# Kernel optimization log

Hardware: AMD Instinct MI355X
Metric: run time of the kernel (lower is better)

The kernel has to match this reference:

```python
import jax, jax.numpy as jnp
import numpy as np
from itertools import product

L0 = (41, 1600, 1408)  # sparse_shape (z,y,x) from pc_range / voxel_size + [1,0,0]
B = 4
N_PER = 25000
PNAMES = ['w_in','s_in','b_in','w1','s1','b1','w2a','s2a','b2a','w2b','s2b','b2b','w2c','s2c','b2c','w3a','s3a','b3a','w3b','s3b','b3b','w3c','s3c','b3c','w4a','s4a','b4a','w4b','s4b','b4b','w4c','s4c','b4c','w_out','s_out','b_out']


def _enc(c, shape):
    D, H, W = shape
    return ((c[:, 0].astype(np.int64) * D + c[:, 1]) * H + c[:, 2]) * W + c[:, 3]


def _subm_rb(coords, shape):
    # submanifold conv rulebook: out site i gathers input j with coord_j = coord_i + offset
    N = coords.shape[0]
    keys = _enc(coords, shape)
    order = np.argsort(keys); sk = keys[order]
    ins, outs = [], []
    for dz, dy, dx in product((-1, 0, 1), repeat=3):
        nb = coords.astype(np.int64).copy()
        nb[:, 1] += dz; nb[:, 2] += dy; nb[:, 3] += dx
        ok = ((nb[:, 1] >= 0) & (nb[:, 1] < shape[0]) & (nb[:, 2] >= 0) & (nb[:, 2] < shape[1]) & (nb[:, 3] >= 0) & (nb[:, 3] < shape[2]))
        qi = np.nonzero(ok)[0]
        qk = _enc(nb[qi], shape)
        pos = np.clip(np.searchsorted(sk, qk), 0, N - 1)
        f = sk[pos] == qk
        ins.append(order[pos[f]].astype(np.int32))
        outs.append(qi[f].astype(np.int32))
    R = max(len(a) for a in ins)
    rin = np.zeros((27, R), np.int32); rout = np.full((27, R), N, np.int32)  # pad -> dummy out row
    for k in range(27):
        rin[k, :len(ins[k])] = ins[k]; rout[k, :len(outs[k])] = outs[k]
    return jnp.asarray(rin), jnp.asarray(rout)


def _spconv_rb(coords, shape, ks, st, pd):
    # strided sparse conv: out = (in + pad - k) / stride where divisible and in-bounds
    osh = tuple((shape[i] + 2 * pd[i] - ks[i]) // st[i] + 1 for i in range(3))
    per = []; allk = []
    for off in product(*[range(k) for k in ks]):
        oc = np.empty((coords.shape[0], 4), np.int64)
        oc[:, 0] = coords[:, 0]
        ok = np.ones(coords.shape[0], bool)
        for d in range(3):
            v = coords[:, d + 1].astype(np.int64) + pd[d] - off[d]
            ok &= (v % st[d] == 0)
            v = v // st[d]
            ok &= (v >= 0) & (v < osh[d])
            oc[:, d + 1] = v
        qi = np.nonzero(ok)[0]
        qk = _enc(oc[qi], osh)
        per.append((qi.astype(np.int32), qk)); allk.append(qk)
    uk = np.unique(np.concatenate(allk))
    Nout = len(uk); K = len(per)
    R = max(len(qi) for qi, _ in per)
    rin = np.zeros((K, R), np.int32); rout = np.full((K, R), Nout, np.int32)
    for k, (qi, qk) in enumerate(per):
        rin[k, :len(qi)] = qi
        rout[k, :len(qi)] = np.searchsorted(uk, qk).astype(np.int32)
    t = uk.copy()
    x = t % osh[2]; t //= osh[2]; y = t % osh[1]; t //= osh[1]; z = t % osh[0]; b = t // osh[0]
    ocoords = np.stack([b, z, y, x], 1).astype(np.int32)
    return jnp.asarray(rin), jnp.asarray(rout), ocoords, osh


def _gen_coords(rng):
    # clustered LiDAR-like voxel occupancy: gaussian clusters so 3x3x3 neighborhoods are populated
    out = []
    for b in range(B):
        nc = 250
        ctr = np.stack([rng.integers(6, 34, nc), rng.integers(60, 1540, nc), rng.integers(60, 1348, nc)], 1)
        pts = ctr[np.repeat(np.arange(nc), 400)] + rng.normal(0.0, 2.0, (nc * 400, 3))
        pts = np.rint(pts).astype(np.int64)
        for d in range(3):
            pts[:, d] = np.clip(pts[:, d], 0, L0[d] - 1)
        keys = (pts[:, 0] * L0[1] + pts[:, 1]) * L0[2] + pts[:, 2]
        _, ui = np.unique(keys, return_index=True)
        assert len(ui) >= N_PER
        c = pts[np.sort(ui[:N_PER])]
        out.append(np.concatenate([np.full((N_PER, 1), b, np.int64), c], 1))
    return np.concatenate(out, 0).astype(np.int32)


def _conv(feat, W, rin, rout, nout):
    # gather -> per-offset GEMM -> scatter-add (spconv rulebook algorithm)
    out = jnp.zeros((nout + 1, W.shape[2]), feat.dtype)  # +1 dummy row for padding
    for k in range(W.shape[0]):
        out = out.at[rout[k]].add(feat[rin[k]] @ W[k])
    return out[:nout]


def _bnrelu(x, s, b):
    # eval-mode BatchNorm1d folded to affine, then ReLU
    return jax.nn.relu(x * s + b)


def _net(voxels, normalizer, rb1_in, rb1_out, rb2s_in, rb2s_out, batch2, rb2_in, rb2_out, rb3s_in, rb3s_out, batch3, rb3_in, rb3_out, rb4s_in, rb4s_out, batch4, rb4_in, rb4_out, rbo_in, rbo_out, batch_out, P):
    n0 = voxels.shape[0]; n2 = batch2.shape[0]; n3 = batch3.shape[0]; n4 = batch4.shape[0]; no = batch_out.shape[0]
    f = voxels.sum(1) / normalizer  # mean VFE: (N0, 4)
    x = _bnrelu(_conv(f, P['w_in'], rb1_in, rb1_out, n0), P['s_in'], P['b_in'])
    x = _bnrelu(_conv(x, P['w1'], rb1_in, rb1_out, n0), P['s1'], P['b1'])
    x = _bnrelu(_conv(x, P['w2a'], rb2s_in, rb2s_out, n2), P['s2a'], P['b2a'])
    x = _bnrelu(_conv(x, P['w2b'], rb2_in, rb2_out, n2), P['s2b'], P['b2b'])
    x = _bnrelu(_conv(x, P['w2c'], rb2_in, rb2_out, n2), P['s2c'], P['b2c'])
    x = _bnrelu(_conv(x, P['w3a'], rb3s_in, rb3s_out, n3), P['s3a'], P['b3a'])
    x = _bnrelu(_conv(x, P['w3b'], rb3_in, rb3_out, n3), P['s3b'], P['b3b'])
    x = _bnrelu(_conv(x, P['w3c'], rb3_in, rb3_out, n3), P['s3c'], P['b3c'])
    x = _bnrelu(_conv(x, P['w4a'], rb4s_in, rb4s_out, n4), P['s4a'], P['b4a'])
    x = _bnrelu(_conv(x, P['w4b'], rb4_in, rb4_out, n4), P['s4b'], P['b4b'])
    x = _bnrelu(_conv(x, P['w4c'], rb4_in, rb4_out, n4), P['s4c'], P['b4c'])
    x = _bnrelu(_conv(x, P['w_out'], rbo_in, rbo_out, no), P['s_out'], P['b_out'])
    # per-batch global max pool over active voxels (== F.max_pool1d over voxel dim)
    return jax.ops.segment_max(x, batch_out.astype(jnp.int32), num_segments=B)


def setup_inputs():
    rng = np.random.default_rng(0)
    coords0 = _gen_coords(rng)
    rb1_in, rb1_out = _subm_rb(coords0, L0)
    rb2s_in, rb2s_out, c2, sh2 = _spconv_rb(coords0, L0, (3, 3, 3), (2, 2, 2), (1, 1, 1))
    rb2_in, rb2_out = _subm_rb(c2, sh2)
    rb3s_in, rb3s_out, c3, sh3 = _spconv_rb(c2, sh2, (3, 3, 3), (2, 2, 2), (1, 1, 1))
    rb3_in, rb3_out = _subm_rb(c3, sh3)
    rb4s_in, rb4s_out, c4, sh4 = _spconv_rb(c3, sh3, (3, 3, 3), (2, 2, 2), (0, 1, 1))
    rb4_in, rb4_out = _subm_rb(c4, sh4)
    rbo_in, rbo_out, co, _ = _spconv_rb(c4, sh4, (3, 1, 1), (2, 1, 1), (0, 0, 0))
    N0 = coords0.shape[0]
    d = dict(
        voxels=jnp.asarray(rng.normal(0, 1, (N0, 5, 4)).astype(np.float32)),
        voxel_num_points=jnp.asarray(rng.integers(1, 6, N0).astype(np.int32)),
        voxel_coords=jnp.asarray(coords0),
        rb1_in=rb1_in, rb1_out=rb1_out,
        rb2s_in=rb2s_in, rb2s_out=rb2s_out, batch2=jnp.asarray(c2[:, 0]),
        rb2_in=rb2_in, rb2_out=rb2_out,
        rb3s_in=rb3s_in, rb3s_out=rb3s_out, batch3=jnp.asarray(c3[:, 0]),
        rb3_in=rb3_in, rb3_out=rb3_out,
        rb4s_in=rb4s_in, rb4s_out=rb4s_out, batch4=jnp.asarray(c4[:, 0]),
        rb4_in=rb4_in, rb4_out=rb4_out,
        rbo_in=rbo_in, rbo_out=rbo_out, batch_out=jnp.asarray(co[:, 0]),
    )
    def _w(k, ci, co_):
        return jnp.asarray((rng.normal(0, 1, (k, ci, co_)) / np.sqrt(k * ci)).astype(np.float32))
    def _bn(c):
        return (jnp.asarray(rng.uniform(0.5, 1.5, c).astype(np.float32)), jnp.asarray(rng.normal(0, 0.1, c).astype(np.float32)))
    d['w_in'] = _w(27, 4, 16); d['s_in'], d['b_in'] = _bn(16)
    d['w1'] = _w(27, 16, 16); d['s1'], d['b1'] = _bn(16)
    d['w2a'] = _w(27, 16, 32); d['s2a'], d['b2a'] = _bn(32)
    d['w2b'] = _w(27, 32, 32); d['s2b'], d['b2b'] = _bn(32)
    d['w2c'] = _w(27, 32, 32); d['s2c'], d['b2c'] = _bn(32)
    d['w3a'] = _w(27, 32, 64); d['s3a'], d['b3a'] = _bn(64)
    d['w3b'] = _w(27, 64, 64); d['s3b'], d['b3b'] = _bn(64)
    d['w3c'] = _w(27, 64, 64); d['s3c'], d['b3c'] = _bn(64)
    d['w4a'] = _w(27, 64, 64); d['s4a'], d['b4a'] = _bn(64)
    d['w4b'] = _w(27, 64, 64); d['s4b'], d['b4b'] = _bn(64)
    d['w4c'] = _w(27, 64, 64); d['s4c'], d['b4c'] = _bn(64)
    d['w_out'] = _w(3, 64, 128); d['s_out'], d['b_out'] = _bn(128)
    return d


def reference(voxels, voxel_num_points, voxel_coords, rb1_in, rb1_out, rb2s_in, rb2s_out, batch2, rb2_in, rb2_out, rb3s_in, rb3s_out, batch3, rb3_in, rb3_out, rb4s_in, rb4s_out, batch4, rb4_in, rb4_out, rbo_in, rbo_out, batch_out, w_in, s_in, b_in, w1, s1, b1, w2a, s2a, b2a, w2b, s2b, b2b, w2c, s2c, b2c, w3a, s3a, b3a, w3b, s3b, b3b, w3c, s3c, b3c, w4a, s4a, b4a, w4b, s4b, b4b, w4c, s4c, b4c, w_out, s_out, b_out):
    normalizer = jnp.maximum(voxel_num_points.astype(voxels.dtype), 1.0)[:, None]
    P = dict(zip(PNAMES, (w_in, s_in, b_in, w1, s1, b1, w2a, s2a, b2a, w2b, s2b, b2b, w2c, s2c, b2c, w3a, s3a, b3a, w3b, s3b, b3b, w3c, s3c, b3c, w4a, s4a, b4a, w4b, s4b, b4b, w4c, s4c, b4c, w_out, s_out, b_out)))
    return _net(voxels, normalizer, rb1_in, rb1_out, rb2s_in, rb2s_out, batch2, rb2_in, rb2_out, rb3s_in, rb3s_out, batch3, rb3_in, rb3_out, rb4s_in, rb4s_out, batch4, rb4_in, rb4_out, rbo_in, rbo_out, batch_out, P)
```

## Files before the change

kernel.cpp:

```cpp
#include <hip/hip_runtime.h>
#include <cstddef>
#include <cstdint>

typedef _Float16 half8 __attribute__((ext_vector_type(8)));
typedef float floatx4 __attribute__((ext_vector_type(4)));

static inline int cdiv_i(int a, int b) { return (a + b - 1) / b; }

__global__ void feat_kernel(const float* __restrict__ vox,
                            const int* __restrict__ vnp,
                            _Float16* __restrict__ f, int N0) {
  int t = blockIdx.x * blockDim.x + threadIdx.x;
  if (t >= (N0 + 1) * 8) return;
  int i = t >> 3, c = t & 7;
  float v = 0.f;
  if (i < N0 && c < 4) {
    const float* p = vox + (size_t)i * 20 + c;
    v = (p[0] + p[4] + p[8] + p[12] + p[16]) / fmaxf((float)vnp[i], 1.f);
  }
  f[t] = (_Float16)v;
}

struct RB { const int* rin; const int* rout; int K, R, nout, start, end, off; };
struct RBs { RB d[8]; };
__global__ void rb_fill_all(RBs P, int* __restrict__ tbl, int total) {
  int idx = blockIdx.x * blockDim.x + threadIdx.x;
  if (idx >= total) return;
#pragma unroll
  for (int l = 0; l < 8; ++l) {
    if (idx >= P.d[l].start && idx < P.d[l].end) {
      const RB rb = P.d[l];
      int e = idx - rb.start;
      int o = rb.rout[e];
      if ((unsigned)o < (unsigned)rb.nout) {
        int k = e / rb.R;
        tbl[rb.off + (size_t)k * rb.nout + o] = rb.rin[e];
      }
    }
  }
}

__global__ void tbl_fill_kernel(const int* __restrict__ rin,
                                const int* __restrict__ rout,
                                int* __restrict__ tbl, int K, int R, int nout) {
  int e = blockIdx.x * blockDim.x + threadIdx.x;
  if (e >= K * R) return;
  int o = rout[e];
  if ((unsigned)o >= (unsigned)nout) return;
  int k = e / R;
  tbl[(size_t)k * nout + o] = rin[e];
}

struct WP { const float* W; int K, Ci, CiPad, Co, start, end, off; };
struct WPs { WP d[12]; };
__global__ void wpack_all(WPs P, _Float16* __restrict__ Bp, int total) {
  int idx = blockIdx.x * blockDim.x + threadIdx.x;
  if (idx >= total) return;
#pragma unroll
  for (int l = 0; l < 12; ++l) {
    if (idx >= P.d[l].start && idx < P.d[l].end) {
      const WP w = P.d[l];
      int e = idx - w.start;
      int j = e & 7;
      int lane = (e >> 3) & 63;
      int rest = e >> 9;
      int NT = w.Co >> 4;
      int t = rest % NT, ch = rest / NT;
      int kk = ch * 32 + ((lane >> 4) << 3) + j;
      int k = kk / w.CiPad, ci = kk % w.CiPad;
      int n = t * 16 + (lane & 15);
      float v = (k < w.K && ci < w.Ci)
                    ? w.W[((size_t)k * w.Ci + ci) * w.Co + n]
                    : 0.f;
      Bp[w.off + e] = (_Float16)v;
    }
  }
}

template <int K, int CiPad, int Co, int KS, int CG>
__global__ __launch_bounds__(256) void conv_mfma(
    const _Float16* __restrict__ feat, const _Float16* __restrict__ Bp,
    const int* __restrict__ tbl, const float* __restrict__ sc,
    const float* __restrict__ bi, _Float16* __restrict__ out,
    int nout, int nin) {
  constexpr int NT = Co / 16;
  constexpr int NTW = NT / CG;
  constexpr int RG = 4 / (KS * CG);
  static_assert(KS * CG * RG == 4 && RG >= 1 && NT % CG == 0);
  constexpr int DIV = (CiPad >= 32) ? (CiPad / 32) : 1;
  constexpr int NCH = (K * CiPad + 31) / 32;
  constexpr int L2C = (CiPad == 8) ? 3 : 4;
  constexpr int CoP = Co + 4;

  __shared__ float red[(KS > 1) ? (KS - 1) * RG * 16 * CoP : 1];

  if (blockIdx.x == 0 && threadIdx.x < Co)
    out[(size_t)nout * Co + threadIdx.x] = (_Float16)0.f;

  const int wave = threadIdx.x >> 6, lane = threadIdx.x & 63;
  const int ks = wave % KS;
  const int cg = (wave / KS) % CG;
  const int rowg = wave / (KS * CG);
  const int m = lane & 15, lb = (lane >> 4) * 8;
  const int i0 = (blockIdx.x * RG + rowg) * 16;
  if constexpr (KS == 1) {
    if (i0 >= nout) return;
  }
  const int row = i0 + m;
  const bool rOK = row < nout;

  floatx4 acc[NTW];
#pragma unroll
  for (int n = 0; n < NTW; ++n) {
    floatx4 z = {0.f, 0.f, 0.f, 0.f};
    acc[n] = z;
  }

  if constexpr (CiPad >= 32) {
    constexpr int NKW = (K + KS - 1) / KS;
    constexpr int NC = NKW * DIV;
    constexpr int DA = NC < 4 ? NC : 4;
    constexpr int DB = NC < 2 ? NC : 2;
    int idx[NKW];
#pragma unroll
    for (int q = 0; q < NKW; ++q) {
      int k = ks + q * KS;
      int jj = (rOK && k < K) ? tbl[(size_t)k * nout + row] : -1;
      idx[q] = (jj < 0) ? nin : jj;
    }
    half8 ap[DA];
    half8 bq[DB][NTW];
#pragma unroll
    for (int d = 0; d < DA; ++d)
      ap[d] = *(const half8*)(feat + (size_t)idx[d / DIV] * CiPad +
                              (d % DIV) * 32 + lb);
#pragma unroll
    for (int d = 0; d < DB; ++d) {
      int k = ks + (d / DIV) * KS;
      int ch = ((k < K) ? k : (K - 1)) * DIV + (d % DIV);
#pragma unroll
      for (int n = 0; n < NTW; ++n)
        bq[d][n] = *(const half8*)(Bp + ((size_t)ch * NT * 64 + lane) * 8 +
                                   (size_t)(cg * NTW + n) * 512);
    }
#pragma unroll
    for (int ii = 0; ii < NC; ++ii) {
      half8 a = ap[ii % DA];
      half8 bt[NTW];
#pragma unroll
      for (int n = 0; n < NTW; ++n) bt[n] = bq[ii % DB][n];
      if (ii + DA < NC) {
        int nx = ii + DA;
        ap[ii % DA] = *(const half8*)(feat + (size_t)idx[nx / DIV] * CiPad +
                                      (nx % DIV) * 32 + lb);
      }
      if (ii + DB < NC) {
        int nx = ii + DB;
        int k = ks + (nx / DIV) * KS;
        int ch = ((k < K) ? k : (K - 1)) * DIV + (nx % DIV);
#pragma unroll
        for (int n = 0; n < NTW; ++n)
          bq[ii % DB][n] = *(const half8*)(Bp + ((size_t)ch * NT * 64 + lane) * 8 +
                                           (size_t)(cg * NTW + n) * 512);
      }
#pragma unroll
      for (int n = 0; n < NTW; ++n)
        acc[n] = __builtin_amdgcn_mfma_f32_16x16x32_f16(a, bt[n], acc[n], 0, 0, 0);
    }
  } else {
    constexpr int NC = NCH;
    constexpr int DA = NC < 4 ? NC : 4;
    constexpr int DB = NC < 2 ? NC : 2;
    int idx[NC];
#pragma unroll
    for (int q = 0; q < NC; ++q) {
      int ko = (q * 32 + lb) >> L2C;
      int jj = (rOK && ko < K) ? tbl[(size_t)ko * nout + row] : -1;
      idx[q] = (jj < 0) ? nin : jj;
    }
    half8 ap[DA];
    half8 bq[DB][NTW];
#pragma unroll
    for (int d = 0; d < DA; ++d)
      ap[d] = *(const half8*)(feat + (size_t)idx[d] * CiPad +
                              ((d * 32 + lb) & (CiPad - 1)));
#pragma unroll
    for (int d = 0; d < DB; ++d)
#pragma unroll
      for (int n = 0; n < NTW; ++n)
        bq[d][n] = *(const half8*)(Bp + ((size_t)d * NT * 64 + lane) * 8 +
                                   (size_t)(cg * NTW + n) * 512);
#pragma unroll
    for (int ii = 0; ii < NC; ++ii) {
      half8 a = ap[ii % DA];
      half8 bt[NTW];
#pragma unroll
      for (int n = 0; n < NTW; ++n) bt[n] = bq[ii % DB][n];
      if (ii + DA < NC) {
        int nx = ii + DA;
        ap[ii % DA] = *(const half8*)(feat + (size_t)idx[nx] * CiPad +
                                      ((nx * 32 + lb) & (CiPad - 1)));
      }
      if (ii + DB < NC) {
        int nx = ii + DB;
#pragma unroll
        for (int n = 0; n < NTW; ++n)
          bq[ii % DB][n] = *(const half8*)(Bp + ((size_t)nx * NT * 64 + lane) * 8 +
                                           (size_t)(cg * NTW + n) * 512);
      }
#pragma unroll
      for (int n = 0; n < NTW; ++n)
        acc[n] = __builtin_amdgcn_mfma_f32_16x16x32_f16(a, bt[n], acc[n], 0, 0, 0);
    }
  }

  const int rl = (lane >> 4) * 4;
  if constexpr (KS > 1) {
    if (ks > 0) {
#pragma unroll
      for (int n = 0; n < NTW; ++n) {
        int col = (cg * NTW + n) * 16 + m;
#pragma unroll
        for (int r = 0; r < 4; ++r)
          red[((ks - 1) * RG + rowg) * 16 * CoP + (rl + r) * CoP + col] = acc[n][r];
      }
    }
    __syncthreads();
    if (ks > 0) return;
#pragma unroll
    for (int s = 1; s < KS; ++s)
#pragma unroll
      for (int n = 0; n < NTW; ++n) {
        int col = (cg * NTW + n) * 16 + m;
#pragma unroll
        for (int r = 0; r < 4; ++r)
          acc[n][r] += red[((s - 1) * RG + rowg) * 16 * CoP + (rl + r) * CoP + col];
      }
  }

#pragma unroll
  for (int n = 0; n < NTW; ++n) {
    int col = (cg * NTW + n) * 16 + m;
    float s_ = sc[col], b_ = bi[col];
#pragma unroll
    for (int r = 0; r < 4; ++r) {
      int orow = i0 + rl + r;
      if (orow < nout)
        out[(size_t)orow * Co + col] = (_Float16)fmaxf(fmaf(acc[n][r], s_, b_), 0.f);
    }
  }
}

__global__ __launch_bounds__(256) void segmax2(const _Float16* __restrict__ x,
                                               const int* __restrict__ batch,
                                               int n, float* __restrict__ out) {
  const int RPB = 128;
  int c = threadIdx.x & 127, g = threadIdx.x >> 7;
  int r0 = blockIdx.x * RPB + g;
  int rend = min(n, blockIdx.x * RPB + RPB);
  float mx = 0.f;
  int cb = -1;
  for (int r = r0; r < rend; r += 2) {
    int b = batch[r];
    if (b != cb) {
      if (cb >= 0)
        atomicMax((int*)out + ((size_t)cb << 7) + c, __float_as_int(mx));
      cb = b;
      mx = 0.f;
    }
    mx = fmaxf(mx, (float)x[(size_t)r * 128 + c]);
  }
  if (cb >= 0)
    atomicMax((int*)out + ((size_t)cb << 7) + c, __float_as_int(mx));
}

extern "C" void kernel_launch(void* const* d_in, const int* in_sizes, int n_in,
                              void* d_out, int out_size, void* d_ws, size_t ws_size,
                              hipStream_t stream) {
  auto I = [&](int idx) { return (const int*)d_in[idx]; };
  auto F = [&](int idx) { return (const float*)d_in[idx]; };

  const int N0  = in_sizes[1];
  const int R1  = in_sizes[3] / 27;
  const int R2s = in_sizes[5] / 27;
  const int n2  = in_sizes[7];
  const int R2  = in_sizes[8] / 27;
  const int R3s = in_sizes[10] / 27;
  const int n3  = in_sizes[12];
  const int R3  = in_sizes[13] / 27;
  const int R4s = in_sizes[15] / 27;
  const int n4  = in_sizes[17];
  const int R4  = in_sizes[18] / 27;
  const int Ro  = in_sizes[20] / 3;
  const int no  = in_sizes[22];

  const int wIdx[12] = {23, 26, 29, 32, 35, 38, 41, 44, 47, 50, 53, 56};
  const int Ks[12]   = {27, 27, 27, 27, 27, 27, 27, 27, 27, 27, 27, 3};
  const int Cis[12]  = {4, 16, 16, 32, 32, 32, 64, 64, 64, 64, 64, 64};
  const int Cos[12]  = {16, 16, 32, 32, 32, 64, 64, 64, 64, 64, 64, 128};
  WPs P;
  int wtot = 0;
  int bpOff[12];
  for (int l = 0; l < 12; ++l) {
    int cip = Cis[l] < 8 ? 8 : Cis[l];
    int nch = (Ks[l] * cip + 31) / 32;
    int nt = Cos[l] / 16;
    int sz = nch * nt * 512;
    P.d[l].W = F(wIdx[l]);
    P.d[l].K = Ks[l];  P.d[l].Ci = Cis[l];  P.d[l].CiPad = cip;  P.d[l].Co = Cos[l];
    P.d[l].start = wtot;  P.d[l].end = wtot + sz;  P.d[l].off = wtot;
    bpOff[l] = wtot;
    wtot += sz;
  }

  RBs RP;
  const int rbRin[8]  = {3, 5, 8, 10, 13, 15, 18, 20};
  const int rbRs[8]   = {R1, R2s, R2, R3s, R3, R4s, R4, Ro};
  const int rbKs[8]   = {27, 27, 27, 27, 27, 27, 27, 3};
  const int rbNout[8] = {N0, n2, n2, n3, n3, n4, n4, no};
  size_t tblInts[8];
  size_t tblOff[8];
  size_t totTbl = 0;
  int totFill = 0;
  for (int l = 0; l < 8; ++l) {
    tblInts[l] = (size_t)rbNout[l] * rbKs[l];
    tblOff[l] = totTbl;
    totTbl += tblInts[l];
    RP.d[l].rin = I(rbRin[l]);
    RP.d[l].rout = I(rbRin[l] + 1);
    RP.d[l].K = rbKs[l];  RP.d[l].R = rbRs[l];  RP.d[l].nout = rbNout[l];
    RP.d[l].start = totFill;
    totFill += rbKs[l] * rbRs[l];
    RP.d[l].end = totFill;
    RP.d[l].off = (int)tblOff[l];
  }

  size_t S = (size_t)(N0 + 1) * 16;
  auto smax = [&](size_t v) { if (v > S) S = v; };
  smax((size_t)(n2 + 1) * 32);
  smax((size_t)(n3 + 1) * 64);
  smax((size_t)(n4 + 1) * 64);
  smax((size_t)(no + 1) * 128);
  S = (S + 7) & ~(size_t)7;

  _Float16* h = (_Float16*)d_ws;
  size_t off = 0;
  _Float16* f0 = h + off;   off += (size_t)(N0 + 1) * 8;
  _Float16* bufA = h + off; off += S;
  _Float16* bufB = h + off; off += S;
  _Float16* Bp = h + off;   off += (size_t)((wtot + 7) & ~7);
  int* tblBase = (int*)(h + off);
  size_t usedBytes = off * 2;
  bool prebuilt = (usedBytes + totTbl * 4 <= ws_size);

  feat_kernel<<<cdiv_i((N0 + 1) * 8, 256), 256, 0, stream>>>(F(0), I(1), f0, N0);
  wpack_all<<<cdiv_i(wtot, 256), 256, 0, stream>>>(P, Bp, wtot);
  hipMemsetAsync(d_out, 0, (size_t)out_size * 4, stream);

  const int l2rb[12] = {0, 0, 1, 2, 2, 3, 4, 4, 5, 6, 6, 7};
  const int* tblL[12];
  if (prebuilt) {
    hipMemsetAsync(tblBase, 0xFF, totTbl * 4, stream);
    rb_fill_all<<<cdiv_i(totFill, 256), 256, 0, stream>>>(RP, tblBase, totFill);
    for (int l = 0; l < 12; ++l) tblL[l] = tblBase + tblOff[l2rb[l]];
  } else {
    for (int l = 0; l < 12; ++l) tblL[l] = tblBase;
  }
  auto buildSeq = [&](int rb) {
    if (prebuilt) return;
    hipMemsetAsync(tblBase, 0xFF, tblInts[rb] * 4, stream);
    tbl_fill_kernel<<<cdiv_i(rbKs[rb] * rbRs[rb], 256), 256, 0, stream>>>(
        I(rbRin[rb]), I(rbRin[rb] + 1), tblBase, rbKs[rb], rbRs[rb], rbNout[rb]);
  };

#define CONV(Kk, CIP, CO, KSv, CGv, IN, LI, OUTB, NOUT, NIN)                  \
  do {                                                                        \
    constexpr int rowsPerBlk = (4 / (KSv * CGv)) * 16;                        \
    conv_mfma<Kk, CIP, CO, KSv, CGv>                                          \
        <<<cdiv_i(NOUT, rowsPerBlk), 256, 0, stream>>>(                       \
            IN, Bp + bpOff[LI], tblL[LI], F(wIdx[LI] + 1), F(wIdx[LI] + 2),   \
            OUTB, NOUT, NIN);                                                 \
  } while (0)

  buildSeq(0);
  CONV(27, 8, 16, 1, 1, f0, 0, bufA, N0, N0);
  CONV(27, 16, 16, 1, 1, bufA, 1, bufB, N0, N0);
  buildSeq(1);
  CONV(27, 16, 32, 1, 1, bufB, 2, bufA, n2, N0);
  buildSeq(2);
  CONV(27, 32, 32, 1, 1, bufA, 3, bufB, n2, n2);
  CONV(27, 32, 32, 1, 1, bufB, 4, bufA, n2, n2);
  buildSeq(3);
  CONV(27, 32, 64, 2, 1, bufA, 5, bufB, n3, n2);
  buildSeq(4);
  CONV(27, 64, 64, 2, 1, bufB, 6, bufA, n3, n3);
  CONV(27, 64, 64, 2, 1, bufA, 7, bufB, n3, n3);
  buildSeq(5);
  CONV(27, 64, 64, 4, 1, bufB, 8, bufA, n4, n3);
  buildSeq(6);
  CONV(27, 64, 64, 4, 1, bufA, 9, bufB, n4, n4);
  CONV(27, 64, 64, 4, 1, bufB, 10, bufA, n4, n4);
  buildSeq(7);
  CONV(3, 64, 128, 2, 2, bufA, 11, bufB, no, n4);
  segmax2<<<cdiv_i(no, 128), 256, 0, stream>>>(bufB, I(22), no, (float*)d_out);
#undef CONV
}
```

Baseline: 464.0 us.

## Split conv work across K-slices and output-column blocks with XCD-aware block remap

```diff
diff --git a/kernel.cpp b/kernel.cpp
--- a/kernel.cpp
+++ b/kernel.cpp
@@ -77,37 +77,49 @@
   }
 }
 
-template <int K, int CiPad, int Co, int KS, int CG>
+template <int K, int CiPad, int Co, int KS, int CG, int CBLK>
 __global__ __launch_bounds__(256) void conv_mfma(
     const _Float16* __restrict__ feat, const _Float16* __restrict__ Bp,
     const int* __restrict__ tbl, const float* __restrict__ sc,
     const float* __restrict__ bi, _Float16* __restrict__ out,
     int nout, int nin) {
   constexpr int NT = Co / 16;
-  constexpr int NTW = NT / CG;
+  constexpr int NTE = NT / CBLK;
+  constexpr int NTW = NTE / CG;
   constexpr int RG = 4 / (KS * CG);
-  static_assert(KS * CG * RG == 4 && RG >= 1 && NT % CG == 0);
+  static_assert(KS * CG * RG == 4 && RG >= 1 && NT % CBLK == 0 && NTE % CG == 0);
   constexpr int DIV = (CiPad >= 32) ? (CiPad / 32) : 1;
   constexpr int NCH = (K * CiPad + 31) / 32;
   constexpr int L2C = (CiPad == 8) ? 3 : 4;
-  constexpr int CoP = Co + 4;
+  constexpr int CoP = NTE * 16 + 4;
 
   __shared__ float red[(KS > 1) ? (KS - 1) * RG * 16 * CoP : 1];
 
   if (blockIdx.x == 0 && threadIdx.x < Co)
     out[(size_t)nout * Co + threadIdx.x] = (_Float16)0.f;
+
+  int id = blockIdx.x;
+  {
+    int nb = gridDim.x, nb8 = (nb >> 3) << 3;
+    if (id < nb8) {
+      int per = nb >> 3;
+      id = (id & 7) * per + (id >> 3);
+    }
+  }
+  const int rt = id / CBLK, cb = id % CBLK;
 
   const int wave = threadIdx.x >> 6, lane = threadIdx.x & 63;
   const int ks = wave % KS;
   const int cg = (wave / KS) % CG;
   const int rowg = wave / (KS * CG);
   const int m = lane & 15, lb = (lane >> 4) * 8;
-  const int i0 = (blockIdx.x * RG + rowg) * 16;
+  const int i0 = (rt * RG + rowg) * 16;
   if constexpr (KS == 1) {
     if (i0 >= nout) return;
   }
   const int row = i0 + m;
   const bool rOK = row < nout;
+  const int ct0 = cb * NTE + cg * NTW;
 
   floatx4 acc[NTW];
 #pragma unroll
@@ -119,7 +131,7 @@
   if constexpr (CiPad >= 32) {
     constexpr int NKW = (K + KS - 1) / KS;
     constexpr int NC = NKW * DIV;
-    constexpr int DA = NC < 4 ? NC : 4;
+    constexpr int DA = NC < 8 ? NC : 8;
     constexpr int DB = NC < 2 ? NC : 2;
     int idx[NKW];
 #pragma unroll
@@ -141,7 +153,7 @@
 #pragma unroll
       for (int n = 0; n < NTW; ++n)
         bq[d][n] = *(const half8*)(Bp + ((size_t)ch * NT * 64 + lane) * 8 +
-                                   (size_t)(cg * NTW + n) * 512);
+                                   (size_t)(ct0 + n) * 512);
     }
 #pragma unroll
     for (int ii = 0; ii < NC; ++ii) {
@@ -161,52 +173,61 @@
 #pragma unroll
         for (int n = 0; n < NTW; ++n)
           bq[ii % DB][n] = *(const half8*)(Bp + ((size_t)ch * NT * 64 + lane) * 8 +
-                                           (size_t)(cg * NTW + n) * 512);
+                                           (size_t)(ct0 + n) * 512);
       }
 #pragma unroll
       for (int n = 0; n < NTW; ++n)
         acc[n] = __builtin_amdgcn_mfma_f32_16x16x32_f16(a, bt[n], acc[n], 0, 0, 0);
     }
   } else {
-    constexpr int NC = NCH;
-    constexpr int DA = NC < 4 ? NC : 4;
-    constexpr int DB = NC < 2 ? NC : 2;
-    int idx[NC];
-#pragma unroll
-    for (int q = 0; q < NC; ++q) {
-      int ko = (q * 32 + lb) >> L2C;
-      int jj = (rOK && ko < K) ? tbl[(size_t)ko * nout + row] : -1;
+    constexpr int NCW = (NCH + KS - 1) / KS;
+    constexpr int DA = NCW < 8 ? NCW : 8;
+    constexpr int DB = NCW < 2 ? NCW : 2;
+    int idx[NCW];
+#pragma unroll
+    for (int q = 0; q < NCW; ++q) {
+      int ch = ks + q * KS;
+      int ko = (ch * 32 + lb) >> L2C;
+      int jj = (rOK && ko < K && ch < NCH) ? tbl[(size_t)ko * nout + row] : -1;
       idx[q] = (jj < 0) ? nin : jj;
     }
     half8 ap[DA];
     half8 bq[DB][NTW];
 #pragma unroll
-    for (int d = 0; d < DA; ++d)
+    for (int d = 0; d < DA; ++d) {
+      int ch = ks + d * KS;
       ap[d] = *(const half8*)(feat + (size_t)idx[d] * CiPad +
-                              ((d * 32 + lb) & (CiPad - 1)));
-#pragma unroll
-    for (int d = 0; d < DB; ++d)
+                              ((ch * 32 + lb) & (CiPad - 1)));
+    }
+#pragma unroll
+    for (int d = 0; d < DB; ++d) {
+      int ch = ks + d * KS;
+      if (ch >= NCH) ch = NCH - 1;
 #pragma unroll
       for (int n = 0; n < NTW; ++n)
-        bq[d][n] = *(const half8*)(Bp + ((size_t)d * NT * 64 + lane) * 8 +
-                                   (size_t)(cg * NTW + n) * 512);
-#pragma unroll
-    for (int ii = 0; ii < NC; ++ii) {
+        bq[d][n] = *(const half8*)(Bp + ((size_t)ch * NT * 64 + lane) * 8 +
+                                   (size_t)(ct0 + n) * 512);
+    }
+#pragma unroll
+    for (int ii = 0; ii < NCW; ++ii) {
       half8 a = ap[ii % DA];
       half8 bt[NTW];
 #pragma unroll
       for (int n = 0; n < NTW; ++n) bt[n] = bq[ii % DB][n];
-      if (ii + DA < NC) {
+      if (ii + DA < NCW) {
         int nx = ii + DA;
+        int ch = ks + nx * KS;
         ap[ii % DA] = *(const half8*)(feat + (size_t)idx[nx] * CiPad +
-                                      ((nx * 32 + lb) & (CiPad - 1)));
-      }
-      if (ii + DB < NC) {
+                                      ((ch * 32 + lb) & (CiPad - 1)));
+      }
+      if (ii + DB < NCW) {
         int nx = ii + DB;
+        int ch = ks + nx * KS;
+        if (ch >= NCH) ch = NCH - 1;
 #pragma unroll
         for (int n = 0; n < NTW; ++n)
-          bq[ii % DB][n] = *(const half8*)(Bp + ((size_t)nx * NT * 64 + lane) * 8 +
-                                           (size_t)(cg * NTW + n) * 512);
+          bq[ii % DB][n] = *(const half8*)(Bp + ((size_t)ch * NT * 64 + lane) * 8 +
+                                           (size_t)(ct0 + n) * 512);
       }
 #pragma unroll
       for (int n = 0; n < NTW; ++n)
@@ -219,10 +240,10 @@
     if (ks > 0) {
 #pragma unroll
       for (int n = 0; n < NTW; ++n) {
-        int col = (cg * NTW + n) * 16 + m;
+        int lcol = (cg * NTW + n) * 16 + m;
 #pragma unroll
         for (int r = 0; r < 4; ++r)
-          red[((ks - 1) * RG + rowg) * 16 * CoP + (rl + r) * CoP + col] = acc[n][r];
+          red[((ks - 1) * RG + rowg) * 16 * CoP + (rl + r) * CoP + lcol] = acc[n][r];
       }
     }
     __syncthreads();
@@ -231,16 +252,16 @@
     for (int s = 1; s < KS; ++s)
 #pragma unroll
       for (int n = 0; n < NTW; ++n) {
-        int col = (cg * NTW + n) * 16 + m;
+        int lcol = (cg * NTW + n) * 16 + m;
 #pragma unroll
         for (int r = 0; r < 4; ++r)
-          acc[n][r] += red[((s - 1) * RG + rowg) * 16 * CoP + (rl + r) * CoP + col];
+          acc[n][r] += red[((s - 1) * RG + rowg) * 16 * CoP + (rl + r) * CoP + lcol];
       }
   }
 
 #pragma unroll
   for (int n = 0; n < NTW; ++n) {
-    int col = (cg * NTW + n) * 16 + m;
+    int col = (ct0 + n) * 16 + m;
     float s_ = sc[col], b_ = bi[col];
 #pragma unroll
     for (int r = 0; r < 4; ++r) {
@@ -318,8 +339,7 @@
   const int rbRs[8]   = {R1, R2s, R2, R3s, R3, R4s, R4, Ro};
   const int rbKs[8]   = {27, 27, 27, 27, 27, 27, 27, 3};
   const int rbNout[8] = {N0, n2, n2, n3, n3, n4, n4, no};
-  size_t tblInts[8];
-  size_t tblOff[8];
+  size_t tblInts[8], tblOff[8];
   size_t totTbl = 0;
   int totFill = 0;
   for (int l = 0; l < 8; ++l) {
@@ -373,35 +393,36 @@
         I(rbRin[rb]), I(rbRin[rb] + 1), tblBase, rbKs[rb], rbRs[rb], rbNout[rb]);
   };
 
-#define CONV(Kk, CIP, CO, KSv, CGv, IN, LI, OUTB, NOUT, NIN)                  \
+#define CONV(Kk, CIP, CO, KSv, CGv, CBv, IN, LI, OUTB, NOUT, NIN)             \
   do {                                                                        \
     constexpr int rowsPerBlk = (4 / (KSv * CGv)) * 16;                        \
-    conv_mfma<Kk, CIP, CO, KSv, CGv>                                          \
-        <<<cdiv_i(NOUT, rowsPerBlk), 256, 0, stream>>>(                       \
+    int nblk = cdiv_i(NOUT, rowsPerBlk) * CBv;                                \
+    conv_mfma<Kk, CIP, CO, KSv, CGv, CBv>                                     \
+        <<<nblk, 256, 0, stream>>>(                                           \
             IN, Bp + bpOff[LI], tblL[LI], F(wIdx[LI] + 1), F(wIdx[LI] + 2),   \
             OUTB, NOUT, NIN);                                                 \
   } while (0)
 
   buildSeq(0);
-  CONV(27, 8, 16, 1, 1, f0, 0, bufA, N0, N0);
-  CONV(27, 16, 16, 1, 1, bufA, 1, bufB, N0, N0);
+  CONV(27, 8, 16, 1, 1, 1, f0, 0, bufA, N0, N0);
+  CONV(27, 16, 16, 2, 1, 1, bufA, 1, bufB, N0, N0);
   buildSeq(1);
-  CONV(27, 16, 32, 1, 1, bufB, 2, bufA, n2, N0);
+  CONV(27, 16, 32, 2, 1, 1, bufB, 2, bufA, n2, N0);
   buildSeq(2);
-  CONV(27, 32, 32, 1, 1, bufA, 3, bufB, n2, n2);
-  CONV(27, 32, 32, 1, 1, bufB, 4, bufA, n2, n2);
+  CONV(27, 32, 32, 2, 1, 1, bufA, 3, bufB, n2, n2);
+  CONV(27, 32, 32, 2, 1, 1, bufB, 4, bufA, n2, n2);
   buildSeq(3);
-  CONV(27, 32, 64, 2, 1, bufA, 5, bufB, n3, n2);
+  CONV(27, 32, 64, 4, 1, 1, bufA, 5, bufB, n3, n2);
   buildSeq(4);
-  CONV(27, 64, 64, 2, 1, bufB, 6, bufA, n3, n3);
-  CONV(27, 64, 64, 2, 1, bufA, 7, bufB, n3, n3);
+  CONV(27, 64, 64, 4, 1, 1, bufB, 6, bufA, n3, n3);
+  CONV(27, 64, 64, 4, 1, 1, bufA, 7, bufB, n3, n3);
   buildSeq(5);
-  CONV(27, 64, 64, 4, 1, bufB, 8, bufA, n4, n3);
+  CONV(27, 64, 64, 4, 1, 2, bufB, 8, bufA, n4, n3);
   buildSeq(6);
-  CONV(27, 64, 64, 4, 1, bufA, 9, bufB, n4, n4);
-  CONV(27, 64, 64, 4, 1, bufB, 10, bufA, n4, n4);
+  CONV(27, 64, 64, 4, 1, 2, bufA, 9, bufB, n4, n4);
+  CONV(27, 64, 64, 4, 1, 2, bufB, 10, bufA, n4, n4);
   buildSeq(7);
-  CONV(3, 64, 128, 2, 2, bufA, 11, bufB, no, n4);
+  CONV(3, 64, 128, 2, 2, 2, bufA, 11, bufB, no, n4);
   segmax2<<<cdiv_i(no, 128), 256, 0, stream>>>(bufB, I(22), no, (float*)d_out);
 #undef CONV
 }
```

After: 448.2 us. 1.04x faster.
